# Optimization experiments

Measured on AMD Instinct MI355X. Metric: run time of the kernel, lower is better.

## Reference

```python
import jax, jax.numpy as jnp
import numpy as np
import math

B, L, D, H = 4, 2048, 1024, 16
HD = D // H


def setup_inputs() -> dict:
    key = jax.random.key(0)
    k1, k2, k3 = jax.random.split(key, 3)
    x = jax.random.normal(k1, (B, L, D), dtype=jnp.float32)
    # Linear weights stored as [in, out] so y = x @ W (equivalent to torch x @ W.T)
    Wqkv = jax.random.normal(k2, (D, 3 * D), dtype=jnp.float32) * (1.0 / math.sqrt(D))
    Wproj = jax.random.normal(k3, (D, D), dtype=jnp.float32) * (1.0 / math.sqrt(D))
    attn_mask = jnp.tril(jnp.ones((L, L), dtype=bool))  # True = attend (causal)
    key_padding_mask = jnp.zeros((B, L), dtype=bool)     # True = padded (none here)
    return {"x": x, "Wqkv": Wqkv, "Wproj": Wproj,
            "attn_mask": attn_mask, "key_padding_mask": key_padding_mask}


def reference(x, Wqkv, Wproj, attn_mask, key_padding_mask):
    Bx, Lx, Dx = x.shape
    qkv = x @ Wqkv                              # [B, L, 3D]
    q, k, v = jnp.split(qkv, 3, axis=-1)
    def shape(t):
        return t.reshape(Bx, Lx, H, HD).transpose(0, 2, 1, 3)  # [B, H, L, hd]
    q, k, v = shape(q), shape(k), shape(v)
    att = jnp.einsum('bhqd,bhkd->bhqk', q, k) / math.sqrt(HD)  # [B, H, L, L]
    neg_inf = jnp.float32(-jnp.inf)
    att = jnp.where(attn_mask[None, None, :, :], att, neg_inf)
    att = jnp.where(key_padding_mask[:, None, None, :], neg_inf, att)
    att = jax.nn.softmax(att, axis=-1)
    y = jnp.einsum('bhqk,bhkd->bhqd', att, v)   # [B, H, L, hd]
    y = y.transpose(0, 2, 1, 3).reshape(Bx, Lx, Dx)
    return y @ Wproj
```

## Files before the change

### kernel.cpp

```cpp
#include <hip/hip_runtime.h>
#include <cstdint>
#include <cstddef>


typedef __attribute__((ext_vector_type(8))) __bf16 bf16x8;
typedef __attribute__((ext_vector_type(4))) __bf16 bf16x4;
typedef __attribute__((ext_vector_type(4))) float f32x4;
typedef __attribute__((ext_vector_type(16))) float f32x16;

__device__ __forceinline__ f32x4 mfma_bf16(bf16x8 a, bf16x8 b, f32x4 c) {
  return __builtin_amdgcn_mfma_f32_16x16x32_bf16(a, b, c, 0, 0, 0);
}

__device__ __forceinline__ f32x16 mfma32(bf16x8 a, bf16x8 b, f32x16 c) {
  return __builtin_amdgcn_mfma_f32_32x32x16_bf16(a, b, c, 0, 0, 0);
}

__device__ __forceinline__ unsigned cvtpk(float a, float b) {
  unsigned r;
  asm("v_cvt_pk_bf16_f32 %0, %1, %2" : "=v"(r) : "v"(a), "v"(b));
  return r;
}

__device__ __forceinline__ void async_copy16(const void* gsrc, void* ldsdst) {
  __builtin_amdgcn_global_load_lds(
      (const __attribute__((address_space(1))) void*)gsrc,
      (__attribute__((address_space(3))) void*)ldsdst, 16, 0, 0);
}

__global__ __launch_bounds__(256) void f32_to_bf16(
    const float* __restrict__ in, __bf16* __restrict__ out) {
  const size_t i = ((size_t)blockIdx.x * 256 + threadIdx.x) * 4;
  const float4 v = *(const float4*)&in[i];
  bf16x4 o = {(__bf16)v.x, (__bf16)v.y, (__bf16)v.z, (__bf16)v.w};
  *(bf16x4*)&out[i] = o;
}

__global__ __launch_bounds__(256) void transpose_f32_bf16(
    const float* __restrict__ in, __bf16* __restrict__ out, int R, int C) {
  __shared__ float tile[32][33];
  const int c0 = blockIdx.x * 32;
  const int r0 = blockIdx.y * 32;
  const int tx = threadIdx.x & 31;
  const int ty = threadIdx.x >> 5;
#pragma unroll
  for (int i = 0; i < 32; i += 8)
    tile[ty + i][tx] = in[(size_t)(r0 + ty + i) * C + c0 + tx];
  __syncthreads();
#pragma unroll
  for (int i = 0; i < 32; i += 8)
    out[(size_t)(c0 + ty + i) * R + r0 + tx] = (__bf16)tile[tx][ty + i];
}


#define GEMM128x256_CORE(Aptr, Bptr)                                         \
  const int srow = tid >> 3;                                      \
  const int schunk = ((tid & 7) ^ (srow & 7)) << 3;                          \
  const __bf16* aBase = &(Aptr)[(size_t)(m0 + srow) * 1024 + schunk];        \
  const __bf16* bBase = &(Bptr)[(size_t)(n0 + srow) * 1024 + schunk];        \
  auto stgTile = [&](int kt, int b3) {                                       \
    __bf16* dst = smem + b3 * 24576 + wave * 512;                            \
    async_copy16(aBase + kt * 64, dst);                                      \
    async_copy16(aBase + 65536 + kt * 64, dst + 4096);                       \
    _Pragma("unroll") for (int u = 0; u < 4; ++u)                            \
        async_copy16(bBase + (size_t)u * 65536 + kt * 64,                    \
                     dst + 8192 + u * 4096);                                 \
  };                                                                         \
  const f32x4 zero = {0.f, 0.f, 0.f, 0.f};                                   \
  f32x4 acc[4][4];                                                           \
  _Pragma("unroll") for (int i = 0; i < 4; ++i)                              \
      _Pragma("unroll") for (int j = 0; j < 4; ++j) acc[i][j] = zero;        \
  stgTile(0, 0);                                                             \
  stgTile(1, 1);                                                             \
  asm volatile("s_waitcnt vmcnt(6)" ::: "memory");      \
  __builtin_amdgcn_s_barrier();                                              \
  for (int t = 0; t < 16; ++t) {                                             \
    const __bf16* As = smem + (t % 3) * 24576;                               \
    const __bf16* Bs = As + 8192;                                            \
    bf16x8 af[4][2], bfr[4][2];                                              \
    _Pragma("unroll") for (int mt = 0; mt < 4; ++mt)                         \
        _Pragma("unroll") for (int kk = 0; kk < 2; ++kk) af[mt][kk] =        \
            *(const bf16x8*)&As[(wr * 64 + mt * 16 + n16) * 64 +             \
                                (((kk * 4 + quad) ^ (n16 & 7)) << 3)];       \
    _Pragma("unroll") for (int nt = 0; nt < 4; ++nt)                         \
        _Pragma("unroll") for (int kk = 0; kk < 2; ++kk) bfr[nt][kk] =       \
            *(const bf16x8*)&Bs[(wc * 64 + nt * 16 + n16) * 64 +             \
                                (((kk * 4 + quad) ^ (n16 & 7)) << 3)];       \
    stgTile((t + 2) & 15, (t + 2) % 3);           \
    __builtin_amdgcn_s_barrier();                                            \
    asm volatile("s_waitcnt lgkmcnt(0)" ::: "memory");                       \
    __builtin_amdgcn_sched_barrier(0);                                       \
    __builtin_amdgcn_s_setprio(1);                                           \
    _Pragma("unroll") for (int mt = 0; mt < 4; ++mt)                         \
        _Pragma("unroll") for (int nt = 0; nt < 4; ++nt)                     \
            _Pragma("unroll") for (int kk = 0; kk < 2; ++kk)                 \
                acc[mt][nt] = mfma_bf16(af[mt][kk], bfr[nt][kk],             \
                                        acc[mt][nt]);                        \
    __builtin_amdgcn_s_setprio(0);                                           \
    asm volatile("s_waitcnt vmcnt(6)" ::: "memory");     \
    __builtin_amdgcn_s_barrier();                                            \
  }                                                                          \
  asm volatile("s_waitcnt vmcnt(0)" ::: "memory");        \
  __builtin_amdgcn_s_barrier();

__global__ __launch_bounds__(512, 2) void gemm_qkv(
    const __bf16* __restrict__ A, const __bf16* __restrict__ BT,
    __bf16* __restrict__ Q, __bf16* __restrict__ Kh, __bf16* __restrict__ VT) {
  extern __shared__ __bf16 smem[];
  const int wg = (blockIdx.x & 7) * 96 + (blockIdx.x >> 3);
  const int bm = wg / 12;
  const int bn = wg % 12;
  const int m0 = bm << 7;
  const int n0 = bn << 8;
  const int tid = threadIdx.x;
  const int wave = tid >> 6;
  const int lane = tid & 63;
  const int n16 = lane & 15;
  const int quad = lane >> 4;
  const int wr = wave >> 2;
  const int wc = wave & 3;

  GEMM128x256_CORE(A, BT)

  __bf16* tw = smem + wave * 2048;
  const int b = m0 >> 11;
  const int l0w = (m0 & 2047) + wr * 64;
  const int n = n0 + wc * 64;

  if (n < 2048) {
    const float QSCALE = 0.125f * 1.44269504089f;
    const bool isQ = (n < 1024);
    const int h = (n & 1023) >> 6;
    __bf16* dst = isQ ? Q : Kh;
    const size_t base = ((size_t)(b * 16 + h) * 2048) * 64;
#pragma unroll
    for (int pass = 0; pass < 2; ++pass) {
#pragma unroll
      for (int mt = 2 * pass; mt < 2 * pass + 2; ++mt) {
#pragma unroll
        for (int nt = 0; nt < 4; ++nt)
#pragma unroll
          for (int r = 0; r < 4; ++r) {
            const int hd = nt * 16 + n16;
            const int mm = (mt & 1) * 16 + quad * 4 + r;
            const float v = isQ ? acc[mt][nt][r] * QSCALE : acc[mt][nt][r];
            tw[mm * 64 + (((hd >> 3) ^ (mm & 7)) << 3) + (hd & 7)] =
                (__bf16)v;
          }
      }
#pragma unroll
      for (int i = 0; i < 4; ++i) {
        const int c = lane + 64 * i;
        const int row = c >> 3;
        const int hd0 = (c & 7) << 3;
        const int phys = (c & 7) ^ (row & 7);
        const bf16x8 v = *(const bf16x8*)&tw[row * 64 + phys * 8];
        *(bf16x8*)&dst[base + (size_t)(l0w + pass * 32 + row) * 64 + hd0] = v;
      }
    }
  } else {
    const int h = (n - 2048) >> 6;
    const size_t bhead = (size_t)(b * 16 + h);
#pragma unroll
    for (int pass = 0; pass < 2; ++pass) {
#pragma unroll
      for (int nt = 2 * pass; nt < 2 * pass + 2; ++nt) {
#pragma unroll
        for (int mt = 0; mt < 4; ++mt)
#pragma unroll
          for (int r = 0; r < 4; ++r) {
            const int hdp = (nt & 1) * 16 + n16;
            const int mm = mt * 16 + quad * 4 + r;
            const int phys = (mm >> 3) ^ (hdp & 7);
            tw[hdp * 64 + phys * 8 + (mm & 7)] = (__bf16)acc[mt][nt][r];
          }
      }
#pragma unroll
      for (int i = 0; i < 4; ++i) {
        const int c = lane + 64 * i;
        const int row = c >> 3;
        const int phys = (c & 7) ^ (row & 7);
        const bf16x8 v = *(const bf16x8*)&tw[row * 64 + phys * 8];
        *(bf16x8*)&VT[(bhead * 64 + pass * 32 + row) * 2048 + l0w +
                      (c & 7) * 8] = v;
      }
    }
  }
}

__global__ __launch_bounds__(512, 2) void gemm_bt_f32out(
    const __bf16* __restrict__ A, const __bf16* __restrict__ BT,
    float* __restrict__ C) {
  extern __shared__ __bf16 smem[];
  const int wg = (blockIdx.x & 7) * 32 + (blockIdx.x >> 3);
  const int bm = wg >> 2;
  const int bn = wg & 3;
  const int m0 = bm << 7;
  const int n0 = bn << 8;
  const int tid = threadIdx.x;
  const int wave = tid >> 6;
  const int lane = tid & 63;
  const int n16 = lane & 15;
  const int quad = lane >> 4;
  const int wr = wave >> 2;
  const int wc = wave & 3;

  GEMM128x256_CORE(A, BT)

#pragma unroll
  for (int mt = 0; mt < 4; ++mt) {
#pragma unroll
    for (int r = 0; r < 4; ++r) {
      const int m = m0 + wr * 64 + mt * 16 + quad * 4 + r;
#pragma unroll
      for (int nt = 0; nt < 4; ++nt) {
        const int nn = n0 + wc * 64 + nt * 16 + n16;
        C[(size_t)m * 1024 + nn] = acc[mt][nt][r];
      }
    }
  }
}

__global__ __launch_bounds__(256, 2) void flash_attn(
    const __bf16* __restrict__ Q, const __bf16* __restrict__ Kh,
    const __bf16* __restrict__ VT, __bf16* __restrict__ Y) {
  __shared__ __bf16 Ks[2][64 * 64];
  __shared__ __bf16 Vs[2][64 * 64];
  const int bh = blockIdx.x;
  const int p = blockIdx.y;
  const int tid = threadIdx.x;
  const int wave = tid >> 6;
  const int lane = tid & 63;
  const int lrow = lane & 31;
  const int hi = lane >> 5;
  const int lswz = lane & 7;
  const __bf16* Qb = Q + (size_t)bh * 2048 * 64;
  const __bf16* Kb = Kh + (size_t)bh * 2048 * 64;
  const __bf16* Vb = VT + (size_t)bh * 64 * 2048;
  const int b = bh >> 4;
  const int h = bh & 15;
  const f32x16 zero16 = {0.f, 0.f, 0.f, 0.f, 0.f, 0.f, 0.f, 0.f,
                         0.f, 0.f, 0.f, 0.f, 0.f, 0.f, 0.f, 0.f};

  const int srow = tid >> 3;
  const int sswz = ((tid & 7) ^ (srow & 7)) << 3;
  const size_t kg0 = (size_t)srow * 64 + sswz;
  const size_t kg1 = (size_t)(srow + 32) * 64 + sswz;
  const size_t vg0 = (size_t)srow * 2048 + sswz;
  const size_t vg1 = (size_t)(srow + 32) * 2048 + sswz;
  const int ldst0 = wave * 512;
  const int ldst1 = 2048 + wave * 512;

#pragma unroll
  for (int tt = 0; tt < 2; ++tt) {
    const int t = tt ? 15 - p : p;
    const int q0w = t * 128 + wave * 32;
    const int myq = q0w + lrow;

    bf16x8 qf[4];
#pragma unroll
    for (int i = 0; i < 4; ++i)
      qf[i] = *(const bf16x8*)&Qb[(size_t)myq * 64 + i * 16 + hi * 8];

    f32x16 o0 = zero16, o1 = zero16;
    float lsum = 0.f;
    const int nsteps = 2 * (t + 1);

    __syncthreads();
    async_copy16(&Kb[kg0], &Ks[0][ldst0]);
    async_copy16(&Kb[kg1], &Ks[0][ldst1]);
    async_copy16(&Vb[vg0], &Vs[0][ldst0]);
    async_copy16(&Vb[vg1], &Vs[0][ldst1]);

    for (int kt = 0; kt < nsteps; ++kt) {
      const int buf = kt & 1;
      const int c0 = kt << 6;
      __syncthreads();
      if (kt + 1 < nsteps) {
        const int nb = buf ^ 1;
        const int cn = c0 + 64;
        async_copy16(&Kb[kg0 + (size_t)cn * 64], &Ks[nb][ldst0]);
        async_copy16(&Kb[kg1 + (size_t)cn * 64], &Ks[nb][ldst1]);
        async_copy16(&Vb[vg0 + cn], &Vs[nb][ldst0]);
        async_copy16(&Vb[vg1 + cn], &Vs[nb][ldst1]);
      }
      if (c0 > q0w + 31) continue;

      const __bf16* ks = Ks[buf];
      const __bf16* vs = Vs[buf];

      f32x16 sc[2];
#pragma unroll
      for (int ch = 0; ch < 2; ++ch) {
        sc[ch] = zero16;
#pragma unroll
        for (int i = 0; i < 4; ++i) {
          const bf16x8 kf = *(const bf16x8*)&ks[(ch * 32 + lrow) * 64 +
                                                (((2 * i + hi) ^ lswz) << 3)];
          sc[ch] = mfma32(kf, qf[i], sc[ch]);
        }
      }
      if (c0 + 63 > q0w) {
#pragma unroll
        for (int ch = 0; ch < 2; ++ch)
#pragma unroll
          for (int r = 0; r < 16; ++r) {
            const int k = c0 + ch * 32 + (r & 3) + 8 * (r >> 2) + 4 * hi;
            float e = __builtin_amdgcn_exp2f(sc[ch][r]);
            e = (k <= myq) ? e : 0.f;
            sc[ch][r] = e;
            lsum += e;
          }
      } else {
#pragma unroll
        for (int ch = 0; ch < 2; ++ch)
#pragma unroll
          for (int r = 0; r < 16; ++r) {
            const float e = __builtin_amdgcn_exp2f(sc[ch][r]);
            sc[ch][r] = e;
            lsum += e;
          }
      }
#pragma unroll
      for (int ch = 0; ch < 2; ++ch) {
#pragma unroll
        for (int kc = 0; kc < 2; ++kc) {
          unsigned c01 = cvtpk(sc[ch][kc * 8 + 0], sc[ch][kc * 8 + 1]);
          unsigned c23 = cvtpk(sc[ch][kc * 8 + 2], sc[ch][kc * 8 + 3]);
          unsigned c45 = cvtpk(sc[ch][kc * 8 + 4], sc[ch][kc * 8 + 5]);
          unsigned c67 = cvtpk(sc[ch][kc * 8 + 6], sc[ch][kc * 8 + 7]);
          asm("v_permlane32_swap_b32 %0, %1" : "+v"(c01), "+v"(c45));
          asm("v_permlane32_swap_b32 %0, %1" : "+v"(c23), "+v"(c67));
          union {
            unsigned u[4];
            bf16x8 v;
          } pu;
          pu.u[0] = c01;
          pu.u[1] = c23;
          pu.u[2] = c45;
          pu.u[3] = c67;
          const int kch = ch * 4 + kc * 2 + hi;
          {
            const bf16x8 vf0 = *(const bf16x8*)&vs[(0 * 32 + lrow) * 64 +
                                                   ((kch ^ lswz) << 3)];
            o0 = mfma32(pu.v, vf0, o0);
            const bf16x8 vf1 = *(const bf16x8*)&vs[(1 * 32 + lrow) * 64 +
                                                   ((kch ^ lswz) << 3)];
            o1 = mfma32(pu.v, vf1, o1);
          }
        }
      }
    }

    lsum += __shfl_xor(lsum, 32);
    const float inv = 1.0f / lsum;
    float invr[16];
#pragma unroll
    for (int r = 0; r < 16; ++r)
      invr[r] = __shfl(inv, (r & 3) + 8 * (r >> 2) + 4 * hi);
#pragma unroll
    for (int r = 0; r < 16; ++r) {
      const int row = q0w + (r & 3) + 8 * (r >> 2) + 4 * hi;
      const size_t yb = (size_t)(b * 2048 + row) * 1024 + h * 64;
      Y[yb + lrow] = (__bf16)(o0[r] * invr[r]);
      Y[yb + 32 + lrow] = (__bf16)(o1[r] * invr[r]);
    }
  }
}

extern "C" void kernel_launch(void* const* d_in, const int* in_sizes, int n_in,
                              void* d_out, int out_size, void* d_ws,
                              size_t ws_size, hipStream_t stream) {
  const float* x = (const float*)d_in[0];
  const float* Wqkv = (const float*)d_in[1];
  const float* Wproj = (const float*)d_in[2];
  float* out = (float*)d_out;

  char* ws = (char*)d_ws;
  __bf16* xb = (__bf16*)ws;     ws += (size_t)8192 * 1024 * 2;
  __bf16* WqkvT = (__bf16*)ws;  ws += (size_t)3072 * 1024 * 2;
  __bf16* WprojT = (__bf16*)ws; ws += (size_t)1024 * 1024 * 2;
  __bf16* Qs = (__bf16*)ws;     ws += (size_t)64 * 2048 * 64 * 2;
  __bf16* Ks = (__bf16*)ws;     ws += (size_t)64 * 2048 * 64 * 2;
  __bf16* VTs = (__bf16*)ws;    ws += (size_t)64 * 64 * 2048 * 2;
  __bf16* attn = xb;

  static bool attrSet = false;
  if (!attrSet) {
    hipFuncSetAttribute((const void*)gemm_qkv,
                        hipFuncAttributeMaxDynamicSharedMemorySize, 147456);
    hipFuncSetAttribute((const void*)gemm_bt_f32out,
                        hipFuncAttributeMaxDynamicSharedMemorySize, 147456);
    attrSet = true;
  }

  f32_to_bf16<<<8192, 256, 0, stream>>>(x, xb);
  transpose_f32_bf16<<<dim3(96, 32), 256, 0, stream>>>(Wqkv, WqkvT, 1024, 3072);
  transpose_f32_bf16<<<dim3(32, 32), 256, 0, stream>>>(Wproj, WprojT, 1024, 1024);
  gemm_qkv<<<768, 512, 147456, stream>>>(xb, WqkvT, Qs, Ks, VTs);
  flash_attn<<<dim3(64, 8), 256, 0, stream>>>(Qs, Ks, VTs, attn);
  gemm_bt_f32out<<<256, 512, 147456, stream>>>(attn, WprojT, out);
}
```

Baseline: 239.5 us.

## Shrink GEMM tiles to 128x128 with double buffering and 256-thread blocks

Both GEMM kernels move from 128x256 tiles with 512 threads and a triple-buffered LDS pipeline to 128x128 tiles with 256 threads and a double buffer, waiting for all loads each step. The intent is to double the block count for better CU load balance and cut LDS use from 144KB to 64KB. The cost is less operand reuse per block, more global traffic, and less latency hiding, since each step now waits for all loads to finish.

```diff
diff --git a/kernel.cpp b/kernel.cpp
--- a/kernel.cpp
+++ b/kernel.cpp
@@ -52,30 +52,28 @@
     out[(size_t)(c0 + ty + i) * R + r0 + tx] = (__bf16)tile[tx][ty + i];
 }
 
-
-#define GEMM128x256_CORE(Aptr, Bptr)                                         \
-  const int srow = tid >> 3;                                      \
-  const int schunk = ((tid & 7) ^ (srow & 7)) << 3;                          \
-  const __bf16* aBase = &(Aptr)[(size_t)(m0 + srow) * 1024 + schunk];        \
-  const __bf16* bBase = &(Bptr)[(size_t)(n0 + srow) * 1024 + schunk];        \
-  auto stgTile = [&](int kt, int b3) {                                       \
-    __bf16* dst = smem + b3 * 24576 + wave * 512;                            \
-    async_copy16(aBase + kt * 64, dst);                                      \
-    async_copy16(aBase + 65536 + kt * 64, dst + 4096);                       \
+#define GEMM128x128_CORE(Aptr, Bptr)                                         \
+  const int srow32 = tid >> 3;                                    \
+  const int schunk = ((tid & 7) ^ (srow32 & 7)) << 3;                        \
+  const __bf16* aBase = &(Aptr)[(size_t)(m0 + srow32) * 1024 + schunk];      \
+  const __bf16* bBase = &(Bptr)[(size_t)(n0 + srow32) * 1024 + schunk];      \
+  auto stgTile = [&](int kt, int b2) {                                       \
+    __bf16* dst = smem + b2 * 16384 + wave * 512;                            \
     _Pragma("unroll") for (int u = 0; u < 4; ++u)                            \
-        async_copy16(bBase + (size_t)u * 65536 + kt * 64,                    \
-                     dst + 8192 + u * 4096);                                 \
+        async_copy16(aBase + (size_t)u * 32768 + kt * 64, dst + u * 2048);   \
+    _Pragma("unroll") for (int u = 0; u < 4; ++u)                            \
+        async_copy16(bBase + (size_t)u * 32768 + kt * 64,                    \
+                     dst + 8192 + u * 2048);                                 \
   };                                                                         \
   const f32x4 zero = {0.f, 0.f, 0.f, 0.f};                                   \
   f32x4 acc[4][4];                                                           \
   _Pragma("unroll") for (int i = 0; i < 4; ++i)                              \
       _Pragma("unroll") for (int j = 0; j < 4; ++j) acc[i][j] = zero;        \
   stgTile(0, 0);                                                             \
-  stgTile(1, 1);                                                             \
-  asm volatile("s_waitcnt vmcnt(6)" ::: "memory");      \
+  asm volatile("s_waitcnt vmcnt(0)" ::: "memory");                           \
   __builtin_amdgcn_s_barrier();                                              \
   for (int t = 0; t < 16; ++t) {                                             \
-    const __bf16* As = smem + (t % 3) * 24576;                               \
+    const __bf16* As = smem + (t & 1) * 16384;                               \
     const __bf16* Bs = As + 8192;                                            \
     bf16x8 af[4][2], bfr[4][2];                                              \
     _Pragma("unroll") for (int mt = 0; mt < 4; ++mt)                         \
@@ -86,7 +84,7 @@
         _Pragma("unroll") for (int kk = 0; kk < 2; ++kk) bfr[nt][kk] =       \
             *(const bf16x8*)&Bs[(wc * 64 + nt * 16 + n16) * 64 +             \
                                 (((kk * 4 + quad) ^ (n16 & 7)) << 3)];       \
-    stgTile((t + 2) & 15, (t + 2) % 3);           \
+    if (t < 15) stgTile(t + 1, (t + 1) & 1);                                 \
     __builtin_amdgcn_s_barrier();                                            \
     asm volatile("s_waitcnt lgkmcnt(0)" ::: "memory");                       \
     __builtin_amdgcn_sched_barrier(0);                                       \
@@ -97,30 +95,28 @@
                 acc[mt][nt] = mfma_bf16(af[mt][kk], bfr[nt][kk],             \
                                         acc[mt][nt]);                        \
     __builtin_amdgcn_s_setprio(0);                                           \
-    asm volatile("s_waitcnt vmcnt(6)" ::: "memory");     \
+    asm volatile("s_waitcnt vmcnt(0)" ::: "memory");                         \
     __builtin_amdgcn_s_barrier();                                            \
-  }                                                                          \
-  asm volatile("s_waitcnt vmcnt(0)" ::: "memory");        \
-  __builtin_amdgcn_s_barrier();
-
-__global__ __launch_bounds__(512, 2) void gemm_qkv(
+  }
+
+__global__ __launch_bounds__(256, 2) void gemm_qkv(
     const __bf16* __restrict__ A, const __bf16* __restrict__ BT,
     __bf16* __restrict__ Q, __bf16* __restrict__ Kh, __bf16* __restrict__ VT) {
   extern __shared__ __bf16 smem[];
-  const int wg = (blockIdx.x & 7) * 96 + (blockIdx.x >> 3);
-  const int bm = wg / 12;
-  const int bn = wg % 12;
+  const int wg = (blockIdx.x & 7) * 192 + (blockIdx.x >> 3);
+  const int bm = wg / 24;
+  const int bn = wg % 24;
   const int m0 = bm << 7;
-  const int n0 = bn << 8;
+  const int n0 = bn << 7;
   const int tid = threadIdx.x;
   const int wave = tid >> 6;
   const int lane = tid & 63;
   const int n16 = lane & 15;
   const int quad = lane >> 4;
-  const int wr = wave >> 2;
-  const int wc = wave & 3;
-
-  GEMM128x256_CORE(A, BT)
+  const int wr = wave >> 1;
+  const int wc = wave & 1;
+
+  GEMM128x128_CORE(A, BT)
 
   __bf16* tw = smem + wave * 2048;
   const int b = m0 >> 11;
@@ -188,24 +184,24 @@
   }
 }
 
-__global__ __launch_bounds__(512, 2) void gemm_bt_f32out(
+__global__ __launch_bounds__(256, 2) void gemm_bt_f32out(
     const __bf16* __restrict__ A, const __bf16* __restrict__ BT,
     float* __restrict__ C) {
   extern __shared__ __bf16 smem[];
-  const int wg = (blockIdx.x & 7) * 32 + (blockIdx.x >> 3);
-  const int bm = wg >> 2;
-  const int bn = wg & 3;
+  const int wg = (blockIdx.x & 7) * 64 + (blockIdx.x >> 3);
+  const int bm = wg >> 3;
+  const int bn = wg & 7;
   const int m0 = bm << 7;
-  const int n0 = bn << 8;
+  const int n0 = bn << 7;
   const int tid = threadIdx.x;
   const int wave = tid >> 6;
   const int lane = tid & 63;
   const int n16 = lane & 15;
   const int quad = lane >> 4;
-  const int wr = wave >> 2;
-  const int wc = wave & 3;
-
-  GEMM128x256_CORE(A, BT)
+  const int wr = wave >> 1;
+  const int wc = wave & 1;
+
+  GEMM128x128_CORE(A, BT)
 
 #pragma unroll
   for (int mt = 0; mt < 4; ++mt) {
@@ -388,16 +384,16 @@
   static bool attrSet = false;
   if (!attrSet) {
     hipFuncSetAttribute((const void*)gemm_qkv,
-                        hipFuncAttributeMaxDynamicSharedMemorySize, 147456);
+                        hipFuncAttributeMaxDynamicSharedMemorySize, 65536);
     hipFuncSetAttribute((const void*)gemm_bt_f32out,
-                        hipFuncAttributeMaxDynamicSharedMemorySize, 147456);
+                        hipFuncAttributeMaxDynamicSharedMemorySize, 65536);
     attrSet = true;
   }
 
   f32_to_bf16<<<8192, 256, 0, stream>>>(x, xb);
   transpose_f32_bf16<<<dim3(96, 32), 256, 0, stream>>>(Wqkv, WqkvT, 1024, 3072);
   transpose_f32_bf16<<<dim3(32, 32), 256, 0, stream>>>(Wproj, WprojT, 1024, 1024);
-  gemm_qkv<<<768, 512, 147456, stream>>>(xb, WqkvT, Qs, Ks, VTs);
+  gemm_qkv<<<1536, 256, 65536, stream>>>(xb, WqkvT, Qs, Ks, VTs);
   flash_attn<<<dim3(64, 8), 256, 0, stream>>>(Qs, Ks, VTs, attn);
-  gemm_bt_f32out<<<256, 512, 147456, stream>>>(attn, WprojT, out);
-}
+  gemm_bt_f32out<<<512, 256, 65536, stream>>>(attn, WprojT, out);
+}
```

Result: faster. 227.7 us (-4.9%).
